# Kernel tuning notes

Hardware: AMD Instinct MI355X
Metric: run time of the kernel (lower is better)

## Reference

```python
import jax, jax.numpy as jnp
import numpy as np

W = 10       # workspace_size
ORDER = 2    # quantum-neuron order
STAGES = 2
N_QUBITS = W + ORDER
N_IN = 6     # number of input lanes (len(input))
BATCH = 512


def ry_mat(theta):
    # real rY(theta) = [[cos(t/2), -sin(t/2)], [sin(t/2), cos(t/2)]]
    c = jnp.cos(theta / 2)
    s = jnp.sin(theta / 2)
    return jnp.stack([jnp.stack([c, -s]), jnp.stack([s, c])])


def apply_1q(psi, G, lane):
    # apply 2x2 gate G to qubit `lane` of psi with shape (B, 2, ..., 2)
    ax = lane + 1
    out = jnp.tensordot(G, psi, axes=((1,), (ax,)))  # contracted axis becomes axis 0
    return jnp.moveaxis(out, 0, ax)


def apply_cry(psi, theta, control, target):
    # controlled-rY(theta): rotate target only in the control==1 half of the state
    axc = control + 1
    psi0, psi1 = jnp.split(psi, 2, axis=axc)  # size-1 control axis kept -> lane indices unchanged
    psi1 = apply_1q(psi1, ry_mat(theta), target)
    return jnp.concatenate([psi0, psi1], axis=axc)


def neuron_apply(psi, theta, outlane):
    # Quantum neuron (Cao et al. / Bausch RQNN), measurement-free recursion of depth ORDER.
    # theta: (W+1,) = W input weights + 1 bias. Ancillas live on lanes W .. W+ORDER-1.
    def rot_block(p, sign):
        for i in range(W):
            p = apply_cry(p, sign * theta[i], i, W)  # crY from workspace lane i onto ancilla 0
        return apply_1q(p, ry_mat(sign * theta[W]), W)  # bias rotation on ancilla 0

    def recurse(p, d, sign):
        if d == 0:
            return rot_block(p, sign)
        t = outlane if d == ORDER else W + d
        p = recurse(p, d - 1, 1.0)
        p = apply_cry(p, sign * np.pi, W + d - 1, t)  # controlled-(iY) = crY(pi); inverse = crY(-pi)
        return recurse(p, d - 1, -1.0)

    return recurse(psi, ORDER, 1.0)


def setup_inputs() -> dict:
    key = jax.random.key(0)
    k1, k2, k3, k4 = jax.random.split(key, 4)
    psi = jax.random.normal(k1, (BATCH,) + (2,) * N_QUBITS, dtype=jnp.float32)
    norm = jnp.sqrt((psi ** 2).sum(axis=tuple(range(1, psi.ndim)), keepdims=True))
    psi = psi / norm  # normalized real quantum state per batch element
    inp = jax.random.randint(k2, (N_IN,), 0, 2)
    unitary_theta = jax.random.normal(k3, (STAGES, W), dtype=jnp.float32)
    neuron_theta = jax.random.normal(k4, (STAGES, W, W + 1), dtype=jnp.float32)
    return {"psi": psi, "inp": inp, "unitary_theta": unitary_theta, "neuron_theta": neuron_theta}


def reference(psi, inp, unitary_theta, neuron_theta):
    # BitFlipLayer: X (axis reversal) on input lanes whose bit is 1
    for l in range(N_IN):
        psi = jnp.where(inp[l] == 1, jnp.flip(psi, axis=l + 1), psi)
    # stages of (UnitaryLayer, then one QuantumNeuronLayer per workspace lane)
    for s in range(STAGES):
        for i in range(W):
            psi = apply_1q(psi, ry_mat(unitary_theta[s, i]), i)
        for out in range(W):
            psi = neuron_apply(psi, neuron_theta[s, out], out)
    # probabilities over the input lanes: marginal |amplitude|^2
    probs = (psi ** 2).sum(axis=tuple(range(N_IN + 1, psi.ndim)))  # (B, 2,...,2) over input lanes
    probs = probs.reshape(psi.shape[0], -1)  # (B, 2**N_IN)
    return probs, psi
```

## Files before the change

### kernel.cpp

```cpp
#include <hip/hip_runtime.h>
#include <math.h>


#define NPLANE 512

__device__ __forceinline__ void m1_apply(const float* v, float* w,
                                         float u, float d, float p) {
    w[0] =  u * v[0] - d * v[1] - p * v[2] - p * v[3];
    w[1] =  d * v[0] + u * v[1] + p * v[2] - p * v[3];
    w[2] = -p * v[0] - p * v[1] + d * v[2] - u * v[3];
    w[3] =  p * v[0] - p * v[1] + u * v[2] + d * v[3];
}

__device__ __forceinline__ void m2_apply(float* v, const float* w,
                                         float u, float d, float p) {
    v[0] =  u * w[0] + d * w[1] - p * w[2] + p * w[3];
    v[1] = -d * w[0] + u * w[1] - p * w[2] - p * w[3];
    v[2] = -p * w[0] + p * w[1] + d * w[2] + u * w[3];
    v[3] = -p * w[0] - p * w[1] - u * w[2] + d * w[3];
}

__device__ __forceinline__ void lane_ry(float (&v)[8], int lm, float c, float s, int ln) {
    float ss = (ln & lm) ? s : -s;
#pragma unroll
    for (int r = 0; r < 8; ++r) {
        float p = __shfl_xor(v[r], lm, 64);
        v[r] = c * v[r] + ss * p;
    }
}

__device__ __forceinline__ void wave_ry(float (&v)[8], int wm, float c, float s,
                                        int wv, int ln, float2* buf) {
    const int slot = wv * 64 + ln;
#pragma unroll
    for (int q = 0; q < 4; ++q)
        buf[q * NPLANE + slot] = make_float2(v[2 * q], v[2 * q + 1]);
    __syncthreads();
    const int pslot = (wv ^ wm) * 64 + ln;
    float ss = (wv & wm) ? s : -s;
#pragma unroll
    for (int q = 0; q < 4; ++q) {
        float2 t = buf[q * NPLANE + pslot];
        v[2 * q]     = c * v[2 * q]     + ss * t.x;
        v[2 * q + 1] = c * v[2 * q + 1] + ss * t.y;
    }
}

__global__ __launch_bounds__(512) void rvqe_kernel(
    const float* __restrict__ psi_in,
    const int*   __restrict__ inp,
    const float* __restrict__ ut,
    const float* __restrict__ nt,
    float* __restrict__ out_probs,
    float* __restrict__ out_psi)
{
    __shared__ float2 xbuf[2][4 * NPLANE];

    const int b   = blockIdx.x;
    const int tid = threadIdx.x;
    const int ln  = tid & 63;
    const int wv  = tid >> 6;
    int bi = 0;

    int flip = 0;
#pragma unroll
    for (int l = 0; l < 6; ++l)
        if (inp[l] == 1) flip |= 1 << (5 - l);

    float v[8];
    {
        const float* src = psi_in + (size_t)b * 4096 + (((ln ^ flip) & 63) << 6) + (wv << 3);
        float4 t0 = ((const float4*)src)[0];
        float4 t1 = ((const float4*)src)[1];
        v[0] = t0.x; v[1] = t0.y; v[2] = t0.z; v[3] = t0.w;
        v[4] = t1.x; v[5] = t1.y; v[6] = t1.z; v[7] = t1.w;
    }

    for (int s = 0; s < 2; ++s) {
        const float* uts = ut + s * 10;

#pragma unroll
        for (int i = 0; i < 6; ++i) {
            float cc, ss;
            __sincosf(0.5f * uts[i], &ss, &cc);
            lane_ry(v, 1 << (5 - i), cc, ss, ln);
        }
        {
            float cc, ss;
            __sincosf(0.5f * uts[6], &ss, &cc);
            wave_ry(v, 4, cc, ss, wv, ln, xbuf[bi]); bi ^= 1;
            __sincosf(0.5f * uts[7], &ss, &cc);
            wave_ry(v, 2, cc, ss, wv, ln, xbuf[bi]); bi ^= 1;
            __sincosf(0.5f * uts[8], &ss, &cc);
            wave_ry(v, 1, cc, ss, wv, ln, xbuf[bi]); bi ^= 1;
            __sincosf(0.5f * uts[9], &ss, &cc);
#pragma unroll
            for (int r = 0; r < 4; ++r) {
                float a0 = v[r], a1 = v[r + 4];
                v[r]     = cc * a0 - ss * a1;
                v[r + 4] = ss * a0 + cc * a1;
            }
        }

        for (int out = 0; out < 10; ++out) {
            const float* th = nt + (size_t)(s * 10 + out) * 11;

            float phi = th[10];
#pragma unroll
            for (int i = 0; i < 6; ++i)
                if ((ln >> (5 - i)) & 1) phi += th[i];
            if (wv & 4) phi += th[6];
            if (wv & 2) phi += th[7];
            if (wv & 1) phi += th[8];

            float sA, cA, sB, cB;
            __sincosf(phi, &sA, &cA);
            __sincosf(phi + th[9], &sB, &cB);
            float uA = 0.5f + 0.5f * cA, dA = 0.5f - 0.5f * cA, pA = 0.5f * sA;
            float uB = 0.5f + 0.5f * cB, dB = 0.5f - 0.5f * cB, pB = 0.5f * sB;

            float wA[4], wB[4];
            m1_apply(v,     wA, uA, dA, pA);
            m1_apply(v + 4, wB, uB, dB, pB);

            if (out < 6) {
                const int lm = 1 << (5 - out);
                float ss = (ln & lm) ? 1.f : -1.f;
                wA[1] = ss * __shfl_xor(wA[1], lm, 64);
                wA[3] = ss * __shfl_xor(wA[3], lm, 64);
                wB[1] = ss * __shfl_xor(wB[1], lm, 64);
                wB[3] = ss * __shfl_xor(wB[3], lm, 64);
            } else if (out < 9) {
                const int wm = 1 << (8 - out);
                float2* buf = xbuf[bi]; bi ^= 1;
                const int slot = wv * 64 + ln;
                buf[slot]          = make_float2(wA[1], wA[3]);
                buf[NPLANE + slot] = make_float2(wB[1], wB[3]);
                __syncthreads();
                const int pslot = (wv ^ wm) * 64 + ln;
                float ss = (wv & wm) ? 1.f : -1.f;
                float2 tA = buf[pslot];
                float2 tB = buf[NPLANE + pslot];
                wA[1] = ss * tA.x; wA[3] = ss * tA.y;
                wB[1] = ss * tB.x; wB[3] = ss * tB.y;
            } else {
                float t1 = wA[1], t3 = wA[3];
                wA[1] = -wB[1]; wA[3] = -wB[3];
                wB[1] = t1;     wB[3] = t3;
            }

            m2_apply(v,     wA, uA, dA, pA);
            m2_apply(v + 4, wB, uB, dB, pB);
        }
    }

    float acc = 0.f;
#pragma unroll
    for (int r = 0; r < 8; ++r) acc += v[r] * v[r];
    {
        float* pb = (float*)xbuf[bi];
        pb[wv * 64 + ln] = acc;
        __syncthreads();
        if (wv == 0) {
            float t = 0.f;
#pragma unroll
            for (int w = 0; w < 8; ++w) t += pb[w * 64 + ln];
            out_probs[(size_t)b * 64 + ln] = t;
        }
    }

    float* dst = out_psi + (size_t)b * 4096 + (ln << 6) + (wv << 3);
    ((float4*)dst)[0] = make_float4(v[0], v[1], v[2], v[3]);
    ((float4*)dst)[1] = make_float4(v[4], v[5], v[6], v[7]);
}

extern "C" void kernel_launch(void* const* d_in, const int* in_sizes, int n_in,
                              void* d_out, int out_size, void* d_ws, size_t ws_size,
                              hipStream_t stream) {
    const float* psi = (const float*)d_in[0];
    const int*   inp = (const int*)d_in[1];
    const float* ut  = (const float*)d_in[2];
    const float* nt  = (const float*)d_in[3];

    const int B = in_sizes[0] >> 12;
    float* probs = (float*)d_out;
    float* opsi  = probs + (size_t)B * 64;

    rvqe_kernel<<<B, 512, 0, stream>>>(psi, inp, ut, nt, probs, opsi);
}
```

Measured before the change: 91.12 us.

## Use packed float2 math, DPP lane swaps, and wider LDS exchanges in neuron kernel

Amplitudes are now held as 2-wide vectors so the 4x4 neuron matrices and rotations can map to packed FMA instructions. Lane XOR exchanges with masks 1 and 2 use DPP quad permutes instead of ds_bpermute shuffles. Cross-wave exchanges now use float4 LDS accesses, which halves the number of LDS operations, and each neuron is specialised at compile time. Launch bounds now request 4 blocks per CU, which may constrain register allocation.

Result: faster. 85.82 us (-5.8%).

```diff
diff --git a/kernel.cpp b/kernel.cpp
--- a/kernel.cpp
+++ b/kernel.cpp
@@ -2,51 +2,106 @@
 #include <math.h>
 
 
-#define NPLANE 512
-
-__device__ __forceinline__ void m1_apply(const float* v, float* w,
-                                         float u, float d, float p) {
-    w[0] =  u * v[0] - d * v[1] - p * v[2] - p * v[3];
-    w[1] =  d * v[0] + u * v[1] + p * v[2] - p * v[3];
-    w[2] = -p * v[0] - p * v[1] + d * v[2] - u * v[3];
-    w[3] =  p * v[0] - p * v[1] + u * v[2] + d * v[3];
-}
-
-__device__ __forceinline__ void m2_apply(float* v, const float* w,
-                                         float u, float d, float p) {
-    v[0] =  u * w[0] + d * w[1] - p * w[2] + p * w[3];
-    v[1] = -d * w[0] + u * w[1] - p * w[2] - p * w[3];
-    v[2] = -p * w[0] + p * w[1] + d * w[2] + u * w[3];
-    v[3] = -p * w[0] - p * w[1] - u * w[2] + d * w[3];
-}
-
-__device__ __forceinline__ void lane_ry(float (&v)[8], int lm, float c, float s, int ln) {
-    float ss = (ln & lm) ? s : -s;
-#pragma unroll
-    for (int r = 0; r < 8; ++r) {
-        float p = __shfl_xor(v[r], lm, 64);
-        v[r] = c * v[r] + ss * p;
-    }
-}
-
-__device__ __forceinline__ void wave_ry(float (&v)[8], int wm, float c, float s,
-                                        int wv, int ln, float2* buf) {
+typedef float v2f __attribute__((ext_vector_type(2)));
+
+#define NSLOT 512
+
+__device__ __forceinline__ v2f mk(float a, float b) { v2f r; r.x = a; r.y = b; return r; }
+
+template <int XM>
+__device__ __forceinline__ float shx(float x) {
+    if constexpr (XM == 1) {
+        return __int_as_float(__builtin_amdgcn_update_dpp(
+            0, __float_as_int(x), 0xB1, 0xF, 0xF, true));
+    } else if constexpr (XM == 2) {
+        return __int_as_float(__builtin_amdgcn_update_dpp(
+            0, __float_as_int(x), 0x4E, 0xF, 0xF, true));
+    } else {
+        return __shfl_xor(x, XM, 64);
+    }
+}
+
+template <int LM>
+__device__ __forceinline__ void lane_ry_t(v2f (&V)[4], float c, float s, int ln) {
+    float ss = (ln & LM) ? s : -s;
+#pragma unroll
+    for (int k = 0; k < 4; ++k) {
+        v2f p = mk(shx<LM>(V[k].x), shx<LM>(V[k].y));
+        V[k] = c * V[k] + ss * p;
+    }
+}
+
+__device__ __forceinline__ void wave_ry(v2f (&V)[4], int wm, float c, float s,
+                                        int wv, int ln, float4* buf) {
     const int slot = wv * 64 + ln;
-#pragma unroll
-    for (int q = 0; q < 4; ++q)
-        buf[q * NPLANE + slot] = make_float2(v[2 * q], v[2 * q + 1]);
+    buf[slot]         = make_float4(V[0].x, V[0].y, V[1].x, V[1].y);
+    buf[NSLOT + slot] = make_float4(V[2].x, V[2].y, V[3].x, V[3].y);
     __syncthreads();
     const int pslot = (wv ^ wm) * 64 + ln;
     float ss = (wv & wm) ? s : -s;
-#pragma unroll
-    for (int q = 0; q < 4; ++q) {
-        float2 t = buf[q * NPLANE + pslot];
-        v[2 * q]     = c * v[2 * q]     + ss * t.x;
-        v[2 * q + 1] = c * v[2 * q + 1] + ss * t.y;
-    }
-}
-
-__global__ __launch_bounds__(512) void rvqe_kernel(
+    float4 t0 = buf[pslot];
+    float4 t1 = buf[NSLOT + pslot];
+    V[0] = c * V[0] + ss * mk(t0.x, t0.y);
+    V[1] = c * V[1] + ss * mk(t0.z, t0.w);
+    V[2] = c * V[2] + ss * mk(t1.x, t1.y);
+    V[3] = c * V[3] + ss * mk(t1.z, t1.w);
+}
+
+template <int OUT>
+__device__ __forceinline__ void neuron(v2f (&V)[4], const float* __restrict__ th,
+                                       int wv, int ln, float4* buf) {
+    float a0 = (ln & 32) ? th[0] : 0.f;
+    float a1 = (ln & 16) ? th[1] : 0.f;
+    float a2 = (ln &  8) ? th[2] : 0.f;
+    float a3 = (ln &  4) ? th[3] : 0.f;
+    float a4 = (ln &  2) ? th[4] : 0.f;
+    float a5 = (ln &  1) ? th[5] : 0.f;
+    float wsum = th[10];
+    if (wv & 4) wsum += th[6];
+    if (wv & 2) wsum += th[7];
+    if (wv & 1) wsum += th[8];
+    float phi = ((a0 + a1) + (a2 + a3)) + ((a4 + a5) + wsum);
+
+    float sA, cA, sB, cB;
+    __sincosf(phi, &sA, &cA);
+    __sincosf(phi + th[9], &sB, &cB);
+    float uA = 0.5f + 0.5f * cA, dA = 0.5f - 0.5f * cA, pA = 0.5f * sA;
+    float uB = 0.5f + 0.5f * cB, dB = 0.5f - 0.5f * cB, pB = 0.5f * sB;
+
+    v2f WA01 = mk(uA, dA) * V[0].x + mk(-dA, uA) * V[0].y + mk(-pA, pA) * V[1].x + mk(-pA, -pA) * V[1].y;
+    v2f WA23 = mk(-pA, pA) * V[0].x + mk(-pA, -pA) * V[0].y + mk(dA, uA) * V[1].x + mk(-uA, dA) * V[1].y;
+    v2f WB01 = mk(uB, dB) * V[2].x + mk(-dB, uB) * V[2].y + mk(-pB, pB) * V[3].x + mk(-pB, -pB) * V[3].y;
+    v2f WB23 = mk(-pB, pB) * V[2].x + mk(-pB, -pB) * V[2].y + mk(dB, uB) * V[3].x + mk(-uB, dB) * V[3].y;
+
+    if constexpr (OUT < 6) {
+        constexpr int LM = 1 << (5 - OUT);
+        float ss = (ln & LM) ? 1.f : -1.f;
+        WA01.y = ss * shx<LM>(WA01.y);
+        WA23.y = ss * shx<LM>(WA23.y);
+        WB01.y = ss * shx<LM>(WB01.y);
+        WB23.y = ss * shx<LM>(WB23.y);
+    } else if constexpr (OUT < 9) {
+        constexpr int WM = 1 << (8 - OUT);
+        const int slot = wv * 64 + ln;
+        buf[slot] = make_float4(WA01.y, WA23.y, WB01.y, WB23.y);
+        __syncthreads();
+        const int pslot = (wv ^ WM) * 64 + ln;
+        float ss = (wv & WM) ? 1.f : -1.f;
+        float4 t = buf[pslot];
+        WA01.y = ss * t.x; WA23.y = ss * t.y; WB01.y = ss * t.z; WB23.y = ss * t.w;
+    } else {
+        float t1 = WA01.y, t3 = WA23.y;
+        WA01.y = -WB01.y; WA23.y = -WB23.y;
+        WB01.y = t1;      WB23.y = t3;
+    }
+
+    V[0] = mk(uA, -dA) * WA01.x + mk(dA, uA) * WA01.y + mk(-pA, -pA) * WA23.x + mk(pA, -pA) * WA23.y;
+    V[1] = mk(-pA, -pA) * WA01.x + mk(pA, -pA) * WA01.y + mk(dA, -uA) * WA23.x + mk(uA, dA) * WA23.y;
+    V[2] = mk(uB, -dB) * WB01.x + mk(dB, uB) * WB01.y + mk(-pB, -pB) * WB23.x + mk(pB, -pB) * WB23.y;
+    V[3] = mk(-pB, -pB) * WB01.x + mk(pB, -pB) * WB01.y + mk(dB, -uB) * WB23.x + mk(uB, dB) * WB23.y;
+}
+
+__global__ __launch_bounds__(512, 4) void rvqe_kernel(
     const float* __restrict__ psi_in,
     const int*   __restrict__ inp,
     const float* __restrict__ ut,
@@ -54,7 +109,7 @@
     float* __restrict__ out_probs,
     float* __restrict__ out_psi)
 {
-    __shared__ float2 xbuf[2][4 * NPLANE];
+    __shared__ float4 xbuf[2][2 * NSLOT];
 
     const int b   = blockIdx.x;
     const int tid = threadIdx.x;
@@ -67,98 +122,58 @@
     for (int l = 0; l < 6; ++l)
         if (inp[l] == 1) flip |= 1 << (5 - l);
 
-    float v[8];
+    v2f V[4];
     {
         const float* src = psi_in + (size_t)b * 4096 + (((ln ^ flip) & 63) << 6) + (wv << 3);
         float4 t0 = ((const float4*)src)[0];
         float4 t1 = ((const float4*)src)[1];
-        v[0] = t0.x; v[1] = t0.y; v[2] = t0.z; v[3] = t0.w;
-        v[4] = t1.x; v[5] = t1.y; v[6] = t1.z; v[7] = t1.w;
+        V[0] = mk(t0.x, t0.y); V[1] = mk(t0.z, t0.w);
+        V[2] = mk(t1.x, t1.y); V[3] = mk(t1.z, t1.w);
     }
 
     for (int s = 0; s < 2; ++s) {
         const float* uts = ut + s * 10;
-
-#pragma unroll
-        for (int i = 0; i < 6; ++i) {
-            float cc, ss;
-            __sincosf(0.5f * uts[i], &ss, &cc);
-            lane_ry(v, 1 << (5 - i), cc, ss, ln);
-        }
+        const float* nts = nt + (size_t)s * 110;
+
         {
             float cc, ss;
+            __sincosf(0.5f * uts[0], &ss, &cc); lane_ry_t<32>(V, cc, ss, ln);
+            __sincosf(0.5f * uts[1], &ss, &cc); lane_ry_t<16>(V, cc, ss, ln);
+            __sincosf(0.5f * uts[2], &ss, &cc); lane_ry_t<8>(V, cc, ss, ln);
+            __sincosf(0.5f * uts[3], &ss, &cc); lane_ry_t<4>(V, cc, ss, ln);
+            __sincosf(0.5f * uts[4], &ss, &cc); lane_ry_t<2>(V, cc, ss, ln);
+            __sincosf(0.5f * uts[5], &ss, &cc); lane_ry_t<1>(V, cc, ss, ln);
             __sincosf(0.5f * uts[6], &ss, &cc);
-            wave_ry(v, 4, cc, ss, wv, ln, xbuf[bi]); bi ^= 1;
+            wave_ry(V, 4, cc, ss, wv, ln, xbuf[bi]); bi ^= 1;
             __sincosf(0.5f * uts[7], &ss, &cc);
-            wave_ry(v, 2, cc, ss, wv, ln, xbuf[bi]); bi ^= 1;
+            wave_ry(V, 2, cc, ss, wv, ln, xbuf[bi]); bi ^= 1;
             __sincosf(0.5f * uts[8], &ss, &cc);
-            wave_ry(v, 1, cc, ss, wv, ln, xbuf[bi]); bi ^= 1;
+            wave_ry(V, 1, cc, ss, wv, ln, xbuf[bi]); bi ^= 1;
             __sincosf(0.5f * uts[9], &ss, &cc);
-#pragma unroll
-            for (int r = 0; r < 4; ++r) {
-                float a0 = v[r], a1 = v[r + 4];
-                v[r]     = cc * a0 - ss * a1;
-                v[r + 4] = ss * a0 + cc * a1;
-            }
+            v2f n0 = cc * V[0] - ss * V[2];
+            v2f n2 = ss * V[0] + cc * V[2];
+            v2f n1 = cc * V[1] - ss * V[3];
+            v2f n3 = ss * V[1] + cc * V[3];
+            V[0] = n0; V[1] = n1; V[2] = n2; V[3] = n3;
         }
 
-        for (int out = 0; out < 10; ++out) {
-            const float* th = nt + (size_t)(s * 10 + out) * 11;
-
-            float phi = th[10];
-#pragma unroll
-            for (int i = 0; i < 6; ++i)
-                if ((ln >> (5 - i)) & 1) phi += th[i];
-            if (wv & 4) phi += th[6];
-            if (wv & 2) phi += th[7];
-            if (wv & 1) phi += th[8];
-
-            float sA, cA, sB, cB;
-            __sincosf(phi, &sA, &cA);
-            __sincosf(phi + th[9], &sB, &cB);
-            float uA = 0.5f + 0.5f * cA, dA = 0.5f - 0.5f * cA, pA = 0.5f * sA;
-            float uB = 0.5f + 0.5f * cB, dB = 0.5f - 0.5f * cB, pB = 0.5f * sB;
-
-            float wA[4], wB[4];
-            m1_apply(v,     wA, uA, dA, pA);
-            m1_apply(v + 4, wB, uB, dB, pB);
-
-            if (out < 6) {
-                const int lm = 1 << (5 - out);
-                float ss = (ln & lm) ? 1.f : -1.f;
-                wA[1] = ss * __shfl_xor(wA[1], lm, 64);
-                wA[3] = ss * __shfl_xor(wA[3], lm, 64);
-                wB[1] = ss * __shfl_xor(wB[1], lm, 64);
-                wB[3] = ss * __shfl_xor(wB[3], lm, 64);
-            } else if (out < 9) {
-                const int wm = 1 << (8 - out);
-                float2* buf = xbuf[bi]; bi ^= 1;
-                const int slot = wv * 64 + ln;
-                buf[slot]          = make_float2(wA[1], wA[3]);
-                buf[NPLANE + slot] = make_float2(wB[1], wB[3]);
-                __syncthreads();
-                const int pslot = (wv ^ wm) * 64 + ln;
-                float ss = (wv & wm) ? 1.f : -1.f;
-                float2 tA = buf[pslot];
-                float2 tB = buf[NPLANE + pslot];
-                wA[1] = ss * tA.x; wA[3] = ss * tA.y;
-                wB[1] = ss * tB.x; wB[3] = ss * tB.y;
-            } else {
-                float t1 = wA[1], t3 = wA[3];
-                wA[1] = -wB[1]; wA[3] = -wB[3];
-                wB[1] = t1;     wB[3] = t3;
-            }
-
-            m2_apply(v,     wA, uA, dA, pA);
-            m2_apply(v + 4, wB, uB, dB, pB);
-        }
+        neuron<0>(V, nts + 0 * 11, wv, ln, nullptr);
+        neuron<1>(V, nts + 1 * 11, wv, ln, nullptr);
+        neuron<2>(V, nts + 2 * 11, wv, ln, nullptr);
+        neuron<3>(V, nts + 3 * 11, wv, ln, nullptr);
+        neuron<4>(V, nts + 4 * 11, wv, ln, nullptr);
+        neuron<5>(V, nts + 5 * 11, wv, ln, nullptr);
+        neuron<6>(V, nts + 6 * 11, wv, ln, xbuf[bi]); bi ^= 1;
+        neuron<7>(V, nts + 7 * 11, wv, ln, xbuf[bi]); bi ^= 1;
+        neuron<8>(V, nts + 8 * 11, wv, ln, xbuf[bi]); bi ^= 1;
+        neuron<9>(V, nts + 9 * 11, wv, ln, nullptr);
     }
 
     float acc = 0.f;
 #pragma unroll
-    for (int r = 0; r < 8; ++r) acc += v[r] * v[r];
+    for (int k = 0; k < 4; ++k) acc += V[k].x * V[k].x + V[k].y * V[k].y;
     {
-        float* pb = (float*)xbuf[bi];
+        float* pb = (float*)&xbuf[bi][0];
         pb[wv * 64 + ln] = acc;
         __syncthreads();
         if (wv == 0) {
@@ -170,8 +185,8 @@
     }
 
     float* dst = out_psi + (size_t)b * 4096 + (ln << 6) + (wv << 3);
-    ((float4*)dst)[0] = make_float4(v[0], v[1], v[2], v[3]);
-    ((float4*)dst)[1] = make_float4(v[4], v[5], v[6], v[7]);
+    ((float4*)dst)[0] = make_float4(V[0].x, V[0].y, V[1].x, V[1].y);
+    ((float4*)dst)[1] = make_float4(V[2].x, V[2].y, V[3].x, V[3].y);
 }
 
 extern "C" void kernel_launch(void* const* d_in, const int* in_sizes, int n_in,
```
